# Performance work log

Hardware: AMD Instinct MI355X
Metric: run time of the kernel (lower is better)

Reference implementation:

```python
import jax, jax.numpy as jnp
import numpy as np

B, T, H = 4, 512, 512          # batch, num_target_nodes, hidden
V = 32000                       # static vocab
S, SDV = 512, 300               # source nodes, source dynamic vocab
TDV = 512                       # target dynamic vocab


def setup_inputs() -> dict:
    key = jax.random.key(0)
    ks = jax.random.split(key, 9)
    src_idx = jax.random.randint(ks[6], (B, S), 0, SDV)
    tgt_idx = jax.random.randint(ks[8], (B, T), 0, TDV)
    return {
        "hiddens": jax.random.normal(ks[0], (B, T, H), jnp.float32),
        "Wp": jax.random.normal(ks[1], (H, 3), jnp.float32) * (1.0 / np.sqrt(H)),
        "bp": jnp.zeros((3,), jnp.float32),
        "Wv": jax.random.normal(ks[2], (H, V), jnp.float32) * (1.0 / np.sqrt(H)),
        "bv": jnp.zeros((V,), jnp.float32),
        "source_attentions": jax.nn.softmax(jax.random.normal(ks[3], (B, T, S), jnp.float32), axis=-1),
        "source_attention_maps": jax.nn.one_hot(src_idx, SDV, dtype=jnp.float32),
        "target_attentions": jax.nn.softmax(jax.random.normal(ks[4], (B, T, TDV), jnp.float32), axis=-1),
        "target_attention_maps": jax.nn.one_hot(tgt_idx, TDV, dtype=jnp.float32),
    }


def reference(hiddens, Wp, bp, Wv, bv, source_attentions, source_attention_maps,
              target_attentions, target_attention_maps):
    b, t, h = hiddens.shape
    hf = hiddens.reshape(b * t, h)
    # switch probabilities: [copy_source, copy_target, generate]
    p = jax.nn.softmax(hf @ Wp + bp, axis=1).reshape(b, t, 3)
    p_copy_source = p[..., 0:1]
    p_copy_target = p[..., 1:2]
    p_generate = p[..., 2:3]
    # vocab scores with pad index masked to -inf (vocab_pad_idx = 0)
    scores = hf @ Wv + bv                      # [b*t, V]
    scores = scores.at[:, 0].set(-jnp.inf)
    vocab_probs = jax.nn.softmax(scores.reshape(b, t, -1), axis=-1)
    scaled_vocab_probs = vocab_probs * p_generate
    # copy distributions via one-hot scatter-sum (dense matmul in original)
    scaled_copy_source_probs = jnp.einsum(
        'bts,bsv->btv', source_attentions * p_copy_source, source_attention_maps)
    scaled_copy_target_probs = jnp.einsum(
        'btn,bnv->btv', target_attentions * p_copy_target, target_attention_maps)
    probs = jnp.concatenate(
        [scaled_vocab_probs, scaled_copy_source_probs, scaled_copy_target_probs], axis=2)
    predictions = jnp.argmax(probs, axis=2)
    return (probs, predictions)
```

## Files before the change

### kernel.cpp

```cpp
#include <hip/hip_runtime.h>
#include <hip/hip_bf16.h>
#include <math.h>

#define Bq   4
#define Tq   512
#define Hq   512
#define Vq   32000
#define Sq   512
#define SDVq 300
#define TDVq 512
#define ROWS (Bq * Tq)
#define OUTW (Vq + SDVq + TDVq)

typedef __bf16 bf16x8 __attribute__((ext_vector_type(8)));
typedef float  fx4    __attribute__((ext_vector_type(4)));

__device__ __forceinline__ void async16(const void* g, void* l) {
    __builtin_amdgcn_global_load_lds(
        (const __attribute__((address_space(1))) void*)g,
        (__attribute__((address_space(3))) void*)l, 16, 0, 0);
}

__global__ void compute_p(const float* __restrict__ hiddens,
                          const float* __restrict__ Wp,
                          const float* __restrict__ bp,
                          float* __restrict__ p,
                          float* __restrict__ rowsum) {
    int row  = blockIdx.x;
    int lane = threadIdx.x;
    if (lane == 0) rowsum[row] = 0.f;
    const float* h = hiddens + (size_t)row * Hq;
    float a0 = 0.f, a1 = 0.f, a2 = 0.f;
    for (int i = lane; i < Hq; i += 64) {
        float hv = h[i];
        a0 += hv * Wp[i * 3 + 0];
        a1 += hv * Wp[i * 3 + 1];
        a2 += hv * Wp[i * 3 + 2];
    }
    for (int off = 32; off > 0; off >>= 1) {
        a0 += __shfl_down(a0, off);
        a1 += __shfl_down(a1, off);
        a2 += __shfl_down(a2, off);
    }
    if (lane == 0) {
        float l0 = a0 + bp[0], l1 = a1 + bp[1], l2 = a2 + bp[2];
        float M  = fmaxf(l0, fmaxf(l1, l2));
        float e0 = expf(l0 - M), e1 = expf(l1 - M), e2 = expf(l2 - M);
        float inv = 1.f / (e0 + e1 + e2);
        p[row * 3 + 0] = e0 * inv;
        p[row * 3 + 1] = e1 * inv;
        p[row * 3 + 2] = e2 * inv;
    }
}

__global__ void extract_idx(const float* __restrict__ map, int ncols,
                            int* __restrict__ idx) {
    int row  = blockIdx.x;
    int lane = threadIdx.x;
    const float* r = map + (size_t)row * ncols;
    float best = -1.f; int bi = 0;
    for (int i = lane; i < ncols; i += 64) {
        float v = r[i];
        if (v > best) { best = v; bi = i; }
    }
    for (int off = 32; off > 0; off >>= 1) {
        float ob  = __shfl_down(best, off);
        int   obi = __shfl_down(bi, off);
        if (ob > best) { best = ob; bi = obi; }
    }
    if (lane == 0) idx[row] = bi;
}

__global__ __launch_bounds__(256)
void convert_a(const float* __restrict__ in, __hip_bfloat16* __restrict__ o) {
    int i = blockIdx.x * 256 + threadIdx.x;
    float4 v = ((const float4*)in)[i];
    __hip_bfloat16* op = o + (size_t)i * 4;
    op[0] = __float2bfloat16(v.x);
    op[1] = __float2bfloat16(v.y);
    op[2] = __float2bfloat16(v.z);
    op[3] = __float2bfloat16(v.w);
}

__global__ __launch_bounds__(256)
void transpose_wv(const float* __restrict__ Wv, __hip_bfloat16* __restrict__ Wt) {
    __shared__ float t[32][33];
    int n0 = blockIdx.x * 32, k0 = blockIdx.y * 32;
    int tx = threadIdx.x, ty = threadIdx.y;
#pragma unroll
    for (int r = 0; r < 4; ++r)
        t[ty + r * 8][tx] = Wv[(size_t)(k0 + ty + r * 8) * Vq + n0 + tx];
    __syncthreads();
#pragma unroll
    for (int r = 0; r < 4; ++r)
        Wt[(size_t)(n0 + ty + r * 8) * Hq + k0 + tx] =
            __float2bfloat16(t[tx][ty + r * 8]);
}

__global__ __launch_bounds__(256)
void gemm_mfma(const __hip_bfloat16* __restrict__ A,
               const __hip_bfloat16* __restrict__ Bt,
               const float* __restrict__ bv,
               float* __restrict__ out,
               float* __restrict__ rowsum) {
    __shared__ __align__(16) unsigned short As[3 * 4096];
    __shared__ __align__(16) unsigned short Bs[3 * 4096];
    __shared__ float rs[128];
    int tid  = threadIdx.x;
    int wave = tid >> 6, lane = tid & 63;
    int bm = blockIdx.x * 128;
    int bn = blockIdx.y * 128;
    int wr = wave >> 1, wc = wave & 1;
    int lr = lane & 15;
    int kq = lane >> 4;

    fx4 acc[4][4];
#pragma unroll
    for (int i = 0; i < 4; ++i)
#pragma unroll
        for (int j = 0; j < 4; ++j)
            acc[i][j] = (fx4){0.f, 0.f, 0.f, 0.f};

    int c0 = tid, c1 = tid + 256;
    int ar0 = c0 & 127, ak0 = (c0 >> 7) * 8;
    int ar1 = c1 & 127, ak1 = (c1 >> 7) * 8;
    const unsigned short* Ag = (const unsigned short*)A;
    const unsigned short* Bg = (const unsigned short*)Bt;

#define STAGE(tt, bb) do {                                                   \
        int k0s = (tt) * 32;                                                 \
        unsigned short* Ab = &As[(bb) * 4096 + (wave << 6) * 8];             \
        unsigned short* Bb = &Bs[(bb) * 4096 + (wave << 6) * 8];             \
        async16(Ag + (size_t)(bm + ar0) * Hq + k0s + ak0, Ab);               \
        async16(Ag + (size_t)(bm + ar1) * Hq + k0s + ak1, Ab + 2048);        \
        async16(Bg + (size_t)(bn + ar0) * Hq + k0s + ak0, Bb);               \
        async16(Bg + (size_t)(bn + ar1) * Hq + k0s + ak1, Bb + 2048);        \
    } while (0)

    STAGE(0, 0);
    STAGE(1, 1);

#pragma unroll
    for (int t = 0; t < 16; ++t) {
        if (t < 15) asm volatile("s_waitcnt vmcnt(4)" ::: "memory");
        else        asm volatile("s_waitcnt vmcnt(0)" ::: "memory");
        __builtin_amdgcn_s_barrier();
        asm volatile("" ::: "memory");

        const unsigned short* Asb = &As[(t % 3) * 4096];
        const unsigned short* Bsb = &Bs[(t % 3) * 4096];
        bf16x8 af[4], bfr[4];
#pragma unroll
        for (int i = 0; i < 4; ++i)
            af[i] = *(const bf16x8*)&Asb[(size_t)(kq * 128 + wr * 64 + i * 16 + lr) * 8];
#pragma unroll
        for (int j = 0; j < 4; ++j)
            bfr[j] = *(const bf16x8*)&Bsb[(size_t)(kq * 128 + wc * 64 + j * 16 + lr) * 8];

        if (t + 2 < 16) STAGE(t + 2, (t + 2) % 3);

#pragma unroll
        for (int i = 0; i < 4; ++i)
#pragma unroll
            for (int j = 0; j < 4; ++j)
                acc[i][j] = __builtin_amdgcn_mfma_f32_16x16x32_bf16(
                    af[i], bfr[j], acc[i][j], 0, 0, 0);

        asm volatile("s_waitcnt lgkmcnt(0)" ::: "memory");
    }
#undef STAGE

    if (tid < 128) rs[tid] = 0.f;
    __syncthreads();

    float bvv[4];
#pragma unroll
    for (int j = 0; j < 4; ++j)
        bvv[j] = bv[bn + wc * 64 + j * 16 + lr];

#pragma unroll
    for (int i = 0; i < 4; ++i) {
        int lrow = wr * 64 + i * 16 + kq * 4;
        float rsum[4] = {0.f, 0.f, 0.f, 0.f};
#pragma unroll
        for (int j = 0; j < 4; ++j) {
            int gc = bn + wc * 64 + j * 16 + lr;
#pragma unroll
            for (int r = 0; r < 4; ++r) {
                float v = __expf(acc[i][j][r] + bvv[j]);
                if (gc == 0) v = 0.f;
                out[(size_t)(bm + lrow + r) * OUTW + gc] = v;
                rsum[r] += v;
            }
        }
#pragma unroll
        for (int off = 1; off < 16; off <<= 1) {
#pragma unroll
            for (int r = 0; r < 4; ++r)
                rsum[r] += __shfl_xor(rsum[r], off);
        }
        if (lr == 0) {
#pragma unroll
            for (int r = 0; r < 4; ++r)
                atomicAdd(&rs[lrow + r], rsum[r]);
        }
    }
    __syncthreads();
    if (tid < 128) atomicAdd(&rowsum[bm + tid], rs[tid]);
}

__global__ __launch_bounds__(256)
void scale_rows(float* __restrict__ out, const float* __restrict__ rowsum,
                const float* __restrict__ p,
                float* __restrict__ cval, int* __restrict__ cidx) {
    int row = blockIdx.x;
    int tid = threadIdx.x;
    float* rp = out + (size_t)row * OUTW;
    float scale = p[row * 3 + 2] / rowsum[row];

    const float4* rv = (const float4*)rp;
    float4* wv = (float4*)rp;
    float bm_ = -1.f; int bi = 0;
    for (int i = tid; i < Vq / 4; i += 256) {
        float4 v = rv[i];
        if (v.x > bm_) { bm_ = v.x; bi = i * 4 + 0; }
        if (v.y > bm_) { bm_ = v.y; bi = i * 4 + 1; }
        if (v.z > bm_) { bm_ = v.z; bi = i * 4 + 2; }
        if (v.w > bm_) { bm_ = v.w; bi = i * 4 + 3; }
        v.x *= scale; v.y *= scale; v.z *= scale; v.w *= scale;
        wv[i] = v;
    }
    __shared__ float bs[256];
    __shared__ int   is_[256];
    bs[tid] = bm_; is_[tid] = bi;
    __syncthreads();
    for (int s = 128; s > 0; s >>= 1) {
        if (tid < s) {
            float v2 = bs[tid + s]; int i2 = is_[tid + s];
            if (v2 > bs[tid] || (v2 == bs[tid] && i2 < is_[tid])) {
                bs[tid] = v2; is_[tid] = i2;
            }
        }
        __syncthreads();
    }
    if (tid == 0) { cval[row * 3] = bs[0] * scale; cidx[row * 3] = is_[0]; }
}

__global__ __launch_bounds__(256)
void copy_scatter(const float* __restrict__ att, const int* __restrict__ idx,
                  const float* __restrict__ p, int pcol, int slot,
                  int natt, int nout, float* __restrict__ out, int out_off,
                  float* __restrict__ cval, int* __restrict__ cidx) {
    int row = blockIdx.x;
    int b   = row >> 9;
    int tid = threadIdx.x;
    __shared__ float acc[TDVq];
    for (int i = tid; i < nout; i += 256) acc[i] = 0.f;
    __syncthreads();
    const float* arow = att + (size_t)row * natt;
    const int*   ib   = idx + b * natt;
    for (int s = tid; s < natt; s += 256) {
        atomicAdd(&acc[ib[s]], arow[s]);
    }
    __syncthreads();
    float pc = p[row * 3 + pcol];
    float* orow = out + (size_t)row * OUTW + out_off;
    float bm_ = -INFINITY; int bi = 0;
    for (int v = tid; v < nout; v += 256) {
        float val = acc[v] * pc;
        orow[v] = val;
        if (val > bm_) { bm_ = val; bi = v; }
    }
    __shared__ float bs[256];
    __shared__ int   is_[256];
    bs[tid] = bm_; is_[tid] = bi;
    __syncthreads();
    for (int s = 128; s > 0; s >>= 1) {
        if (tid < s) {
            float v2 = bs[tid + s]; int i2 = is_[tid + s];
            if (v2 > bs[tid] || (v2 == bs[tid] && i2 < is_[tid])) {
                bs[tid] = v2; is_[tid] = i2;
            }
        }
        __syncthreads();
    }
    if (tid == 0) { cval[row * 3 + slot] = bs[0]; cidx[row * 3 + slot] = out_off + is_[0]; }
}

__global__ void combine_pred(const float* __restrict__ cval,
                             const int* __restrict__ cidx,
                             float* __restrict__ pred) {
    int r = blockIdx.x * 256 + threadIdx.x;
    if (r >= ROWS) return;
    float v = cval[r * 3]; int i = cidx[r * 3];
    if (cval[r * 3 + 1] > v) { v = cval[r * 3 + 1]; i = cidx[r * 3 + 1]; }
    if (cval[r * 3 + 2] > v) { v = cval[r * 3 + 2]; i = cidx[r * 3 + 2]; }
    pred[r] = (float)i;
}

extern "C" void kernel_launch(void* const* d_in, const int* in_sizes, int n_in,
                              void* d_out, int out_size, void* d_ws, size_t ws_size,
                              hipStream_t stream) {
    const float* hiddens = (const float*)d_in[0];
    const float* Wp      = (const float*)d_in[1];
    const float* bp      = (const float*)d_in[2];
    const float* Wv      = (const float*)d_in[3];
    const float* bv      = (const float*)d_in[4];
    const float* src_att = (const float*)d_in[5];
    const float* src_map = (const float*)d_in[6];
    const float* tgt_att = (const float*)d_in[7];
    const float* tgt_map = (const float*)d_in[8];

    float* out  = (float*)d_out;
    float* pred = out + (size_t)ROWS * OUTW;

    char* ws = (char*)d_ws;
    float* p_ws   = (float*)(ws);
    int*   sidx   = (int*)(ws + (24 << 10));
    int*   tidx   = (int*)(ws + (32 << 10));
    float* cval   = (float*)(ws + (40 << 10));
    int*   cidx   = (int*)(ws + (64 << 10));
    float* rowsum = (float*)(ws + (88 << 10));
    __hip_bfloat16* A_bf = (__hip_bfloat16*)(ws + (128 << 10));
    __hip_bfloat16* Wt   = (__hip_bfloat16*)(ws + (128 << 10) + (2 << 20));

    convert_a<<<ROWS * Hq / 4 / 256, 256, 0, stream>>>(hiddens, A_bf);
    {
        dim3 tg(Vq / 32, Hq / 32);
        dim3 tb(32, 8);
        transpose_wv<<<tg, tb, 0, stream>>>(Wv, Wt);
    }

    compute_p<<<ROWS, 64, 0, stream>>>(hiddens, Wp, bp, p_ws, rowsum);
    extract_idx<<<Bq * Sq, 64, 0, stream>>>(src_map, SDVq, sidx);
    extract_idx<<<Bq * Tq, 64, 0, stream>>>(tgt_map, TDVq, tidx);

    {
        dim3 gg(ROWS / 128, Vq / 128);
        gemm_mfma<<<gg, 256, 0, stream>>>(A_bf, Wt, bv, out, rowsum);
    }

    scale_rows<<<ROWS, 256, 0, stream>>>(out, rowsum, p_ws, cval, cidx);

    copy_scatter<<<ROWS, 256, 0, stream>>>(src_att, sidx, p_ws, 0, 1, Sq, SDVq,
                                           out, Vq, cval, cidx);
    copy_scatter<<<ROWS, 256, 0, stream>>>(tgt_att, tidx, p_ws, 1, 2, TDVq, TDVq,
                                           out, Vq + SDVq, cval, cidx);

    combine_pred<<<(ROWS + 255) / 256, 256, 0, stream>>>(cval, cidx, pred);
}
```

Baseline: 620.2 us.

## Store GEMM exponentials as bf16 and fuse scale, copy-scatter and argmax into one kernel

The GEMM epilogue writes exp scores to a bf16 scratch buffer instead of fp32 into the output. It also writes per-column-block row partial sums instead of using global atomics, and blocks are remapped so that groups of M-tiles sharing a Wv column tile run together. The prefetch is issued before the LDS fragment reads. A single finalize kernel reduces the partial sums, reads the bf16 exponentials, scales them into the fp32 output, performs both copy scatters and computes the final argmax. This removes several launches and one fp32 read-modify-write pass, at the cost of bf16 rounding of the vocab probabilities, which can change argmax ties.

Measured after the change: 570.2 us. -8.1%, faster.

```diff
diff --git a/kernel.cpp b/kernel.cpp
--- a/kernel.cpp
+++ b/kernel.cpp
@@ -11,9 +11,11 @@
 #define TDVq 512
 #define ROWS (Bq * Tq)
 #define OUTW (Vq + SDVq + TDVq)
+#define NBLK (Vq / 128)
 
 typedef __bf16 bf16x8 __attribute__((ext_vector_type(8)));
 typedef float  fx4    __attribute__((ext_vector_type(4)));
+typedef unsigned short ushort8 __attribute__((ext_vector_type(8)));
 
 __device__ __forceinline__ void async16(const void* g, void* l) {
     __builtin_amdgcn_global_load_lds(
@@ -21,14 +23,18 @@
         (__attribute__((address_space(3))) void*)l, 16, 0, 0);
 }
 
+__device__ __forceinline__ float bf2f(unsigned short u) {
+    union { unsigned int i; float f; } c;
+    c.i = ((unsigned int)u) << 16;
+    return c.f;
+}
+
 __global__ void compute_p(const float* __restrict__ hiddens,
                           const float* __restrict__ Wp,
                           const float* __restrict__ bp,
-                          float* __restrict__ p,
-                          float* __restrict__ rowsum) {
+                          float* __restrict__ p) {
     int row  = blockIdx.x;
     int lane = threadIdx.x;
-    if (lane == 0) rowsum[row] = 0.f;
     const float* h = hiddens + (size_t)row * Hq;
     float a0 = 0.f, a1 = 0.f, a2 = 0.f;
     for (int i = lane; i < Hq; i += 64) {
@@ -101,15 +107,21 @@
 void gemm_mfma(const __hip_bfloat16* __restrict__ A,
                const __hip_bfloat16* __restrict__ Bt,
                const float* __restrict__ bv,
-               float* __restrict__ out,
-               float* __restrict__ rowsum) {
+               __hip_bfloat16* __restrict__ eb,
+               float* __restrict__ partial) {
     __shared__ __align__(16) unsigned short As[3 * 4096];
     __shared__ __align__(16) unsigned short Bs[3 * 4096];
     __shared__ float rs[128];
     int tid  = threadIdx.x;
     int wave = tid >> 6, lane = tid & 63;
-    int bm = blockIdx.x * 128;
-    int bn = blockIdx.y * 128;
+
+    int bid = blockIdx.x;
+    int logical = (bid & 7) * 500 + (bid >> 3);
+    int nb = logical >> 4;
+    int mb = logical & 15;
+    int bm = mb * 128;
+    int bn = nb * 128;
+
     int wr = wave >> 1, wc = wave & 1;
     int lr = lane & 15;
     int kq = lane >> 4;
@@ -147,6 +159,8 @@
         __builtin_amdgcn_s_barrier();
         asm volatile("" ::: "memory");
 
+        if (t + 2 < 16) STAGE(t + 2, (t + 2) % 3);
+
         const unsigned short* Asb = &As[(t % 3) * 4096];
         const unsigned short* Bsb = &Bs[(t % 3) * 4096];
         bf16x8 af[4], bfr[4];
@@ -157,8 +171,6 @@
         for (int j = 0; j < 4; ++j)
             bfr[j] = *(const bf16x8*)&Bsb[(size_t)(kq * 128 + wc * 64 + j * 16 + lr) * 8];
 
-        if (t + 2 < 16) STAGE(t + 2, (t + 2) % 3);
-
 #pragma unroll
         for (int i = 0; i < 4; ++i)
 #pragma unroll
@@ -189,7 +201,7 @@
             for (int r = 0; r < 4; ++r) {
                 float v = __expf(acc[i][j][r] + bvv[j]);
                 if (gc == 0) v = 0.f;
-                out[(size_t)(bm + lrow + r) * OUTW + gc] = v;
+                eb[(size_t)(bm + lrow + r) * Vq + gc] = __float2bfloat16(v);
                 rsum[r] += v;
             }
         }
@@ -206,96 +218,133 @@
         }
     }
     __syncthreads();
-    if (tid < 128) atomicAdd(&rowsum[bm + tid], rs[tid]);
+    if (tid < 128) partial[(size_t)nb * ROWS + bm + tid] = rs[tid];
 }
 
 __global__ __launch_bounds__(256)
-void scale_rows(float* __restrict__ out, const float* __restrict__ rowsum,
-                const float* __restrict__ p,
-                float* __restrict__ cval, int* __restrict__ cidx) {
+void finalize(const __hip_bfloat16* __restrict__ e_bf,
+              const float* __restrict__ partial,
+              const float* __restrict__ p,
+              const float* __restrict__ src_att, const int* __restrict__ sidx,
+              const float* __restrict__ tgt_att, const int* __restrict__ tidx,
+              float* __restrict__ out, float* __restrict__ pred) {
     int row = blockIdx.x;
     int tid = threadIdx.x;
-    float* rp = out + (size_t)row * OUTW;
-    float scale = p[row * 3 + 2] / rowsum[row];
-
-    const float4* rv = (const float4*)rp;
-    float4* wv = (float4*)rp;
-    float bm_ = -1.f; int bi = 0;
-    for (int i = tid; i < Vq / 4; i += 256) {
-        float4 v = rv[i];
-        if (v.x > bm_) { bm_ = v.x; bi = i * 4 + 0; }
-        if (v.y > bm_) { bm_ = v.y; bi = i * 4 + 1; }
-        if (v.z > bm_) { bm_ = v.z; bi = i * 4 + 2; }
-        if (v.w > bm_) { bm_ = v.w; bi = i * 4 + 3; }
-        v.x *= scale; v.y *= scale; v.z *= scale; v.w *= scale;
-        wv[i] = v;
-    }
+    int b   = row >> 9;
+    __shared__ float accs[TDVq];
     __shared__ float bs[256];
     __shared__ int   is_[256];
+    __shared__ float sred[4];
+
+    float s = 0.f;
+    for (int nb = tid; nb < NBLK; nb += 256)
+        s += partial[(size_t)nb * ROWS + row];
+    for (int off = 32; off > 0; off >>= 1) s += __shfl_down(s, off);
+    if ((tid & 63) == 0) sred[tid >> 6] = s;
+    __syncthreads();
+    float S     = sred[0] + sred[1] + sred[2] + sred[3];
+    float scale = p[row * 3 + 2] / S;
+
+    const ushort8* er = (const ushort8*)(e_bf + (size_t)row * Vq);
+    float* orow = out + (size_t)row * OUTW;
+    float4* ov  = (float4*)orow;
+    float bm_ = -1.f; int bi = 0;
+    for (int i = tid; i < Vq / 8; i += 256) {
+        ushort8 v = er[i];
+        float f[8];
+#pragma unroll
+        for (int k = 0; k < 8; ++k) f[k] = bf2f(v[k]);
+#pragma unroll
+        for (int k = 0; k < 8; ++k)
+            if (f[k] > bm_) { bm_ = f[k]; bi = i * 8 + k; }
+        float4 lo = {f[0] * scale, f[1] * scale, f[2] * scale, f[3] * scale};
+        float4 hi = {f[4] * scale, f[5] * scale, f[6] * scale, f[7] * scale};
+        ov[2 * i]     = lo;
+        ov[2 * i + 1] = hi;
+    }
     bs[tid] = bm_; is_[tid] = bi;
     __syncthreads();
-    for (int s = 128; s > 0; s >>= 1) {
-        if (tid < s) {
-            float v2 = bs[tid + s]; int i2 = is_[tid + s];
+    for (int st = 128; st > 0; st >>= 1) {
+        if (tid < st) {
+            float v2 = bs[tid + st]; int i2 = is_[tid + st];
             if (v2 > bs[tid] || (v2 == bs[tid] && i2 < is_[tid])) {
                 bs[tid] = v2; is_[tid] = i2;
             }
         }
         __syncthreads();
     }
-    if (tid == 0) { cval[row * 3] = bs[0] * scale; cidx[row * 3] = is_[0]; }
-}
-
-__global__ __launch_bounds__(256)
-void copy_scatter(const float* __restrict__ att, const int* __restrict__ idx,
-                  const float* __restrict__ p, int pcol, int slot,
-                  int natt, int nout, float* __restrict__ out, int out_off,
-                  float* __restrict__ cval, int* __restrict__ cidx) {
-    int row = blockIdx.x;
-    int b   = row >> 9;
-    int tid = threadIdx.x;
-    __shared__ float acc[TDVq];
-    for (int i = tid; i < nout; i += 256) acc[i] = 0.f;
-    __syncthreads();
-    const float* arow = att + (size_t)row * natt;
-    const int*   ib   = idx + b * natt;
-    for (int s = tid; s < natt; s += 256) {
-        atomicAdd(&acc[ib[s]], arow[s]);
-    }
-    __syncthreads();
-    float pc = p[row * 3 + pcol];
-    float* orow = out + (size_t)row * OUTW + out_off;
-    float bm_ = -INFINITY; int bi = 0;
-    for (int v = tid; v < nout; v += 256) {
-        float val = acc[v] * pc;
-        orow[v] = val;
-        if (val > bm_) { bm_ = val; bi = v; }
-    }
-    __shared__ float bs[256];
-    __shared__ int   is_[256];
-    bs[tid] = bm_; is_[tid] = bi;
-    __syncthreads();
-    for (int s = 128; s > 0; s >>= 1) {
-        if (tid < s) {
-            float v2 = bs[tid + s]; int i2 = is_[tid + s];
+    float cv0 = bs[0] * scale; int ci0 = is_[0];
+    __syncthreads();
+
+    for (int i = tid; i < SDVq; i += 256) accs[i] = 0.f;
+    __syncthreads();
+    {
+        const float* arow = src_att + (size_t)row * Sq;
+        const int*   ib   = sidx + b * Sq;
+        for (int s2 = tid; s2 < Sq; s2 += 256)
+            atomicAdd(&accs[ib[s2]], arow[s2]);
+    }
+    __syncthreads();
+    {
+        float pc = p[row * 3 + 0];
+        float bm2 = -INFINITY; int bi2 = 0;
+        for (int v = tid; v < SDVq; v += 256) {
+            float val = accs[v] * pc;
+            orow[Vq + v] = val;
+            if (val > bm2) { bm2 = val; bi2 = v; }
+        }
+        bs[tid] = bm2; is_[tid] = bi2;
+    }
+    __syncthreads();
+    for (int st = 128; st > 0; st >>= 1) {
+        if (tid < st) {
+            float v2 = bs[tid + st]; int i2 = is_[tid + st];
             if (v2 > bs[tid] || (v2 == bs[tid] && i2 < is_[tid])) {
                 bs[tid] = v2; is_[tid] = i2;
             }
         }
         __syncthreads();
     }
-    if (tid == 0) { cval[row * 3 + slot] = bs[0]; cidx[row * 3 + slot] = out_off + is_[0]; }
-}
-
-__global__ void combine_pred(const float* __restrict__ cval,
-                             const int* __restrict__ cidx,
-                             float* __restrict__ pred) {
-    int r = blockIdx.x * 256 + threadIdx.x;
-    if (r >= ROWS) return;
-    float v = cval[r * 3]; int i = cidx[r * 3];
-    if (cval[r * 3 + 1] > v) { v = cval[r * 3 + 1]; i = cidx[r * 3 + 1]; }
-    if (cval[r * 3 + 2] > v) { v = cval[r * 3 + 2]; i = cidx[r * 3 + 2]; }
-    pred[r] = (float)i;
+    float cv1 = bs[0]; int ci1 = Vq + is_[0];
+    __syncthreads();
+
+    for (int i = tid; i < TDVq; i += 256) accs[i] = 0.f;
+    __syncthreads();
+    {
+        const float* arow = tgt_att + (size_t)row * TDVq;
+        const int*   ib   = tidx + b * TDVq;
+        for (int s2 = tid; s2 < TDVq; s2 += 256)
+            atomicAdd(&accs[ib[s2]], arow[s2]);
+    }
+    __syncthreads();
+    {
+        float pc = p[row * 3 + 1];
+        float bm2 = -INFINITY; int bi2 = 0;
+        for (int v = tid; v < TDVq; v += 256) {
+            float val = accs[v] * pc;
+            orow[Vq + SDVq + v] = val;
+            if (val > bm2) { bm2 = val; bi2 = v; }
+        }
+        bs[tid] = bm2; is_[tid] = bi2;
+    }
+    __syncthreads();
+    for (int st = 128; st > 0; st >>= 1) {
+        if (tid < st) {
+            float v2 = bs[tid + st]; int i2 = is_[tid + st];
+            if (v2 > bs[tid] || (v2 == bs[tid] && i2 < is_[tid])) {
+                bs[tid] = v2; is_[tid] = i2;
+            }
+        }
+        __syncthreads();
+    }
+
+    if (tid == 0) {
+        float cv2 = bs[0]; int ci2 = Vq + SDVq + is_[0];
+        float v = cv0; int i = ci0;
+        if (cv1 > v) { v = cv1; i = ci1; }
+        if (cv2 > v) { v = cv2; i = ci2; }
+        pred[row] = (float)i;
+    }
 }
 
 extern "C" void kernel_launch(void* const* d_in, const int* in_sizes, int n_in,
@@ -315,14 +364,13 @@
     float* pred = out + (size_t)ROWS * OUTW;
 
     char* ws = (char*)d_ws;
-    float* p_ws   = (float*)(ws);
-    int*   sidx   = (int*)(ws + (24 << 10));
-    int*   tidx   = (int*)(ws + (32 << 10));
-    float* cval   = (float*)(ws + (40 << 10));
-    int*   cidx   = (int*)(ws + (64 << 10));
-    float* rowsum = (float*)(ws + (88 << 10));
-    __hip_bfloat16* A_bf = (__hip_bfloat16*)(ws + (128 << 10));
-    __hip_bfloat16* Wt   = (__hip_bfloat16*)(ws + (128 << 10) + (2 << 20));
+    float* p_ws    = (float*)(ws);
+    int*   sidx    = (int*)(ws + (24 << 10));
+    int*   tidx    = (int*)(ws + (32 << 10));
+    float* partial = (float*)(ws + (64 << 10));
+    __hip_bfloat16* A_bf = (__hip_bfloat16*)(ws + (64 << 10) + (2 << 20));
+    __hip_bfloat16* e_bf = (__hip_bfloat16*)(ws + (64 << 10) + (4 << 20));
+    __hip_bfloat16* Wt   = (__hip_bfloat16*)(ws + (64 << 10) + (4 << 20) + (128 << 20));
 
     convert_a<<<ROWS * Hq / 4 / 256, 256, 0, stream>>>(hiddens, A_bf);
     {
@@ -331,21 +379,12 @@
         transpose_wv<<<tg, tb, 0, stream>>>(Wv, Wt);
     }
 
-    compute_p<<<ROWS, 64, 0, stream>>>(hiddens, Wp, bp, p_ws, rowsum);
+    compute_p<<<ROWS, 64, 0, stream>>>(hiddens, Wp, bp, p_ws);
     extract_idx<<<Bq * Sq, 64, 0, stream>>>(src_map, SDVq, sidx);
     extract_idx<<<Bq * Tq, 64, 0, stream>>>(tgt_map, TDVq, tidx);
 
-    {
-        dim3 gg(ROWS / 128, Vq / 128);
-        gemm_mfma<<<gg, 256, 0, stream>>>(A_bf, Wt, bv, out, rowsum);
-    }
-
-    scale_rows<<<ROWS, 256, 0, stream>>>(out, rowsum, p_ws, cval, cidx);
-
-    copy_scatter<<<ROWS, 256, 0, stream>>>(src_att, sidx, p_ws, 0, 1, Sq, SDVq,
-                                           out, Vq, cval, cidx);
-    copy_scatter<<<ROWS, 256, 0, stream>>>(tgt_att, tidx, p_ws, 1, 2, TDVq, TDVq,
-                                           out, Vq + SDVq, cval, cidx);
-
-    combine_pred<<<(ROWS + 255) / 256, 256, 0, stream>>>(cval, cidx, pred);
-}
+    gemm_mfma<<<(ROWS / 128) * NBLK, 256, 0, stream>>>(A_bf, Wt, bv, e_bf, partial);
+
+    finalize<<<ROWS, 256, 0, stream>>>(e_bf, partial, p_ws,
+                                       src_att, sidx, tgt_att, tidx, out, pred);
+}
```
